# Optimization experiments

Measured on AMD Instinct MI355X. Metric: run time of the kernel, lower is better.

## Reference

```python
import jax, jax.numpy as jnp
import numpy as np

N_NODES = 100000


def gcn_conv(x, edge_index, W, b):
    # PyG GCNConv: add self-loops, sym-normalize, linear, scatter-add aggregate
    n = x.shape[0]
    loop = jnp.arange(n, dtype=edge_index.dtype)
    src = jnp.concatenate([edge_index[0], loop])  # [E+N]
    dst = jnp.concatenate([edge_index[1], loop])
    deg = jax.ops.segment_sum(jnp.ones_like(dst, dtype=x.dtype), dst, num_segments=n)
    dinv = jnp.where(deg > 0, jax.lax.rsqrt(deg), 0.0)
    h = x @ W                               # [N, out]
    norm = dinv[src] * dinv[dst]            # [E+N]
    msg = h[src] * norm[:, None]            # [E+N, out]
    out = jax.ops.segment_sum(msg, dst, num_segments=n)
    return out + b


def setup_inputs() -> dict:
    key = jax.random.key(0)
    k1, k2, k3, k4 = jax.random.split(key, 4)
    x = jax.random.normal(k1, (N_NODES, 128), dtype=jnp.float32)
    edge_index = jax.random.randint(k2, (2, 3200000), 0, N_NODES, dtype=jnp.int64)
    W1 = jax.random.normal(k3, (128, 64), dtype=jnp.float32) * (1.0 / np.sqrt(128))
    b1 = jnp.zeros((64,), dtype=jnp.float32)
    W2 = jax.random.normal(k4, (64, 2), dtype=jnp.float32) * (1.0 / np.sqrt(64))
    b2 = jnp.zeros((2,), dtype=jnp.float32)
    return {"x": x, "edge_index": edge_index, "W1": W1, "b1": b1, "W2": W2, "b2": b2}


def reference(x, edge_index, W1, b1, W2, b2):
    h = jax.nn.relu(gcn_conv(x, edge_index, W1, b1))
    return gcn_conv(h, edge_index, W2, b2)
```

## Files before the change

kernel.cpp:

```cpp
#include <hip/hip_runtime.h>
#include <hip/hip_bf16.h>
#include <math.h>

#define N_FEAT 128
#define H1 64
#define H2 2
#define BSHIFT 9
#define BWID (1 << BSHIFT)
#define EPB 8192
#define GR 32

typedef unsigned long long u64;
typedef unsigned int u32;

__device__ __forceinline__ unsigned short f2bf(float f) {
    u32 u = __float_as_uint(f);
    u += 0x7fff + ((u >> 16) & 1);
    return (unsigned short)(u >> 16);
}
__device__ __forceinline__ float bf_lo(u32 v) { return __uint_as_float(v << 16); }
__device__ __forceinline__ float bf_hi(u32 v) { return __uint_as_float(v & 0xffff0000u); }

__device__ __forceinline__ int load_idx(const void* E, size_t i, int is64) {
    if (is64) return (int)((const long long*)E)[i];
    return ((const int*)E)[i];
}

__device__ __forceinline__ int detect_is64(const void* E) {
    const u64* E64 = (const u64*)E;
    return (E64[0] <= 1000000ULL) && (E64[1] <= 1000000ULL) &&
           (E64[2] <= 1000000ULL) && (E64[3] <= 1000000ULL);
}

__global__ __launch_bounds__(256) void k_bcount(const void* __restrict__ E, size_t nE,
                                                int* __restrict__ bcnt, int NB) {
    __shared__ int hist[256];
    __shared__ int s_is64;
    int tid = threadIdx.x;
    hist[tid] = 0;
    if (tid == 0) s_is64 = detect_is64(E);
    __syncthreads();
    int is64 = s_is64;
    size_t e0 = (size_t)blockIdx.x * EPB;
    int cnt = (int)min((size_t)EPB, nE - e0);
    for (int k = tid; k < cnt; k += 256) {
        int d = load_idx(E, nE + e0 + k, is64);
        atomicAdd(&hist[d >> BSHIFT], 1);
    }
    __syncthreads();
    if (tid < NB && hist[tid]) atomicAdd(&bcnt[tid], hist[tid]);
}

__global__ void k_bscan(const int* __restrict__ bcnt, int* __restrict__ boff,
                        u32* __restrict__ gcur, int* __restrict__ rp,
                        int N, int NB, int nE) {
    __shared__ int s[1024];
    int t = threadIdx.x;
    int own = (t < NB) ? bcnt[t] : 0;
    s[t] = own;
    __syncthreads();
    for (int off = 1; off < 1024; off <<= 1) {
        int v = (t >= off) ? s[t - off] : 0;
        __syncthreads();
        s[t] += v;
        __syncthreads();
    }
    int excl = s[t] - own;
    if (t < NB) {
        boff[t] = excl;
        gcur[t] = (u32)excl;
    }
    if (t == 0) {
        boff[NB] = nE;
        rp[N] = nE;
    }
}

__global__ __launch_bounds__(256) void k_bin(const void* __restrict__ E, size_t nE,
                                             u32* __restrict__ gcur,
                                             u32* __restrict__ packed) {
    __shared__ u32 hist[256], lbase[256], lcur[256];
    __shared__ int s_is64;
    int tid = threadIdx.x;
    hist[tid] = 0;
    if (tid == 0) s_is64 = detect_is64(E);
    __syncthreads();
    int is64 = s_is64;
    size_t e0 = (size_t)blockIdx.x * EPB;
    int cnt = (int)min((size_t)EPB, nE - e0);
    for (int k = tid; k < cnt; k += 256) {
        int d = load_idx(E, nE + e0 + k, is64);
        atomicAdd(&hist[d >> BSHIFT], 1u);
    }
    __syncthreads();
    u32 h = hist[tid];
    lbase[tid] = h ? atomicAdd(&gcur[tid], h) : 0u;
    lcur[tid] = 0u;
    __syncthreads();
    for (int k = tid; k < cnt; k += 256) {
        int s = load_idx(E, e0 + k, is64);
        int d = load_idx(E, nE + e0 + k, is64);
        int b = d >> BSHIFT;
        u32 r = atomicAdd(&lcur[b], 1u);
        packed[(size_t)lbase[b] + r] = ((u32)(d & (BWID - 1)) << 17) | (u32)s;
    }
}

__global__ __launch_bounds__(512) void k_csr(const u32* __restrict__ packed,
                                             const int* __restrict__ boff,
                                             int* __restrict__ rp,
                                             float* __restrict__ dinv,
                                             int* __restrict__ col, int N) {
    __shared__ int cnt[BWID];
    __shared__ int cur[BWID];
    __shared__ int s[BWID];
    int tid = threadIdx.x;
    int b = blockIdx.x;
    cnt[tid] = 0;
    __syncthreads();
    int e0 = boff[b], e1 = boff[b + 1];
    for (int e = e0 + tid; e < e1; e += BWID)
        atomicAdd(&cnt[packed[e] >> 17], 1);
    __syncthreads();
    int own = cnt[tid];
    s[tid] = own;
    __syncthreads();
    for (int off = 1; off < BWID; off <<= 1) {
        int v = (tid >= off) ? s[tid - off] : 0;
        __syncthreads();
        s[tid] += v;
        __syncthreads();
    }
    int excl = s[tid] - own;
    int node = b * BWID + tid;
    if (node < N) {
        rp[node] = e0 + excl;
        dinv[node] = rsqrtf((float)(own + 1));
    }
    cur[tid] = excl;
    __syncthreads();
    for (int e = e0 + tid; e < e1; e += BWID) {
        u32 p = packed[e];
        int pos = e0 + atomicAdd(&cur[p >> 17], 1);
        col[pos] = (int)(p & 0x1FFFF);
    }
}

__global__ __launch_bounds__(256) void k_gemm1(const float* __restrict__ x,
                                               const float* __restrict__ W1,
                                               const float* __restrict__ dinv,
                                               unsigned short* __restrict__ h1b, int N) {
    __shared__ float Ws[N_FEAT * H1];
    __shared__ float Xs[GR * N_FEAT];
    int tid = threadIdx.x;
    for (int t = tid; t < N_FEAT * H1 / 4; t += 256)
        ((float4*)Ws)[t] = ((const float4*)W1)[t];
    int row_base = blockIdx.x * GR;
    int nrow = min(GR, N - row_base);
    const float4* xg = (const float4*)(x + (size_t)row_base * N_FEAT);
    int nf4 = nrow * (N_FEAT / 4);
    for (int t = tid; t < nf4; t += 256)
        ((float4*)Xs)[t] = xg[t];
    __syncthreads();

    int lane = tid & 63, wv = tid >> 6;
    int r0 = wv * 8;
    const float4* Xs4 = (const float4*)Xs;
    float acc[8] = {0.f, 0.f, 0.f, 0.f, 0.f, 0.f, 0.f, 0.f};
#pragma unroll 2
    for (int kk = 0; kk < N_FEAT / 4; ++kk) {
        float w0 = Ws[(4 * kk + 0) * H1 + lane];
        float w1 = Ws[(4 * kk + 1) * H1 + lane];
        float w2 = Ws[(4 * kk + 2) * H1 + lane];
        float w3 = Ws[(4 * kk + 3) * H1 + lane];
#pragma unroll
        for (int r = 0; r < 8; ++r) {
            float4 xv = Xs4[(r0 + r) * (N_FEAT / 4) + kk];
            acc[r] = fmaf(xv.x, w0, fmaf(xv.y, w1, fmaf(xv.z, w2, fmaf(xv.w, w3, acc[r]))));
        }
    }
#pragma unroll
    for (int r = 0; r < 8; ++r) {
        int row = row_base + r0 + r;
        if (row < N) h1b[(size_t)row * H1 + lane] = f2bf(acc[r] * dinv[row]);
    }
}

__global__ __launch_bounds__(256) void k_agg1(const u32* __restrict__ h1b32,
                                              const int* __restrict__ rp,
                                              const int* __restrict__ col,
                                              const float* __restrict__ dinv,
                                              const float* __restrict__ b1,
                                              const float* __restrict__ W2,
                                              float2* __restrict__ h2s, int N) {
    int node = blockIdx.x * 4 + (threadIdx.x >> 6);
    int lane = threadIdx.x & 63;
    if (node >= N) return;
    int c2 = lane & 31;
    int h = lane >> 5;
    float a0 = 0.f, a1 = 0.f;
    int e0 = rp[node], e1 = rp[node + 1];
    int deg = e1 - e0;
    int pairs = deg >> 1;
    int p = 0;
    for (; p + 8 <= pairs; p += 8) {
        int idx[8];
        u32 vv[8];
#pragma unroll
        for (int i = 0; i < 8; ++i) idx[i] = col[e0 + 2 * (p + i) + h];
#pragma unroll
        for (int i = 0; i < 8; ++i) vv[i] = h1b32[(size_t)idx[i] * 32 + c2];
#pragma unroll
        for (int i = 0; i < 8; ++i) { a0 += bf_lo(vv[i]); a1 += bf_hi(vv[i]); }
    }
    for (; p < pairs; ++p) {
        int s = col[e0 + 2 * p + h];
        u32 v = h1b32[(size_t)s * 32 + c2];
        a0 += bf_lo(v);
        a1 += bf_hi(v);
    }
    if ((deg & 1) && h == 0) {
        int s = col[e1 - 1];
        u32 v = h1b32[(size_t)s * 32 + c2];
        a0 += bf_lo(v);
        a1 += bf_hi(v);
    }
    a0 += __shfl_xor(a0, 32);
    a1 += __shfl_xor(a1, 32);
    u32 sv = h1b32[(size_t)node * 32 + c2];
    a0 += bf_lo(sv);
    a1 += bf_hi(sv);

    float di = dinv[node];
    float2 bb = ((const float2*)b1)[c2];
    float v0 = fmaxf(fmaf(di, a0, bb.x), 0.f);
    float v1 = fmaxf(fmaf(di, a1, bb.y), 0.f);
    float4 w = ((const float4*)W2)[c2];
    float p0 = fmaf(v0, w.x, v1 * w.z);
    float p1 = fmaf(v0, w.y, v1 * w.w);
#pragma unroll
    for (int off = 16; off; off >>= 1) {
        p0 += __shfl_xor(p0, off);
        p1 += __shfl_xor(p1, off);
    }
    if (lane == 0) h2s[node] = make_float2(di * p0, di * p1);
}

__global__ __launch_bounds__(256) void k_agg2(const float2* __restrict__ h2s,
                                              const int* __restrict__ rp,
                                              const int* __restrict__ col,
                                              const float* __restrict__ dinv,
                                              const float* __restrict__ b2,
                                              float2* __restrict__ out, int N) {
    int g = threadIdx.x >> 4;
    int lane = threadIdx.x & 15;
    int node = blockIdx.x * 16 + g;
    if (node >= N) return;
    int e0 = rp[node], e1 = rp[node + 1];
    float a0 = 0.f, a1 = 0.f;
    for (int e = e0 + lane; e < e1; e += 16) {
        float2 v = h2s[col[e]];
        a0 += v.x;
        a1 += v.y;
    }
#pragma unroll
    for (int off = 8; off; off >>= 1) {
        a0 += __shfl_xor(a0, off, 16);
        a1 += __shfl_xor(a1, off, 16);
    }
    if (lane == 0) {
        float di = dinv[node];
        float2 self = h2s[node];
        out[node] = make_float2(fmaf(di, a0 + self.x, b2[0]),
                                fmaf(di, a1 + self.y, b2[1]));
    }
}

extern "C" void kernel_launch(void* const* d_in, const int* in_sizes, int n_in,
                              void* d_out, int out_size, void* d_ws, size_t ws_size,
                              hipStream_t stream) {
    const float* x  = (const float*)d_in[0];
    const void*  E  = d_in[1];
    const float* W1 = (const float*)d_in[2];
    const float* b1 = (const float*)d_in[3];
    const float* W2 = (const float*)d_in[4];
    const float* b2 = (const float*)d_in[5];
    float2* out = (float2*)d_out;

    const int N  = in_sizes[0] / N_FEAT;
    const int nE = in_sizes[1] / 2;
    const int NB = (N + BWID - 1) / BWID;

    char* ws = (char*)d_ws;
    size_t off = 0;
    auto alloc = [&](size_t bytes) -> void* {
        void* p = ws + off;
        off = (off + bytes + 255) & ~(size_t)255;
        return p;
    };
    int*            bcnt   = (int*)alloc((size_t)NB * 4);
    int*            boff   = (int*)alloc((size_t)(NB + 1) * 4);
    u32*            gcur   = (u32*)alloc((size_t)NB * 4);
    int*            rp     = (int*)alloc((size_t)(N + 1) * 4);
    float*          dinv   = (float*)alloc((size_t)N * 4);
    int*            col    = (int*)alloc((size_t)nE * 4);
    u32*            packed = (u32*)alloc((size_t)nE * 4);
    unsigned short* h1b    = (unsigned short*)alloc((size_t)N * H1 * 2);
    float2*         h2s    = (float2*)alloc((size_t)N * 8);

    hipMemsetAsync(bcnt, 0, (size_t)NB * 4, stream);

    const int cgrid = (nE + EPB - 1) / EPB;

    k_bcount<<<cgrid, 256, 0, stream>>>(E, (size_t)nE, bcnt, NB);
    k_bscan<<<1, 1024, 0, stream>>>(bcnt, boff, gcur, rp, N, NB, nE);
    k_bin<<<cgrid, 256, 0, stream>>>(E, (size_t)nE, gcur, packed);
    k_csr<<<NB, BWID, 0, stream>>>(packed, boff, rp, dinv, col, N);
    k_gemm1<<<(N + GR - 1) / GR, 256, 0, stream>>>(x, W1, dinv, h1b, N);
    k_agg1<<<(N + 3) / 4, 256, 0, stream>>>((const u32*)h1b, rp, col, dinv, b1, W2, h2s, N);
    k_agg2<<<(N + 15) / 16, 256, 0, stream>>>(h2s, rp, col, dinv, b2, out, N);
}
```

Measured before the change: 325.6 us.

## Use 16-byte gathers with 8 edges per wave in agg1; wave-shuffle scan in CSR

The layer-1 aggregation now has each lane load a uint4 (8 bf16 channels), so a 64-lane wave gathers 8 neighbor rows at once instead of 2. Each lane keeps 8 accumulators, and the partial sums are reduced across lane groups with shuffles before the bias, ReLU and W2 projection. The CSR kernel's block-wide Hillis-Steele scan, which needed many __syncthreads, is replaced by a per-wave shuffle scan plus a small shared-memory pass over wave totals. The wider gathers are meant to cut load instructions and expose more memory parallelism, at the cost of more registers and shuffle work per node and a change in summation order.

```diff
diff --git a/kernel.cpp b/kernel.cpp
--- a/kernel.cpp
+++ b/kernel.cpp
@@ -113,8 +113,9 @@
                                              int* __restrict__ col, int N) {
     __shared__ int cnt[BWID];
     __shared__ int cur[BWID];
-    __shared__ int s[BWID];
+    __shared__ int wsum[8];
     int tid = threadIdx.x;
+    int lane = tid & 63, wv = tid >> 6;
     int b = blockIdx.x;
     cnt[tid] = 0;
     __syncthreads();
@@ -123,15 +124,18 @@
         atomicAdd(&cnt[packed[e] >> 17], 1);
     __syncthreads();
     int own = cnt[tid];
-    s[tid] = own;
-    __syncthreads();
-    for (int off = 1; off < BWID; off <<= 1) {
-        int v = (tid >= off) ? s[tid - off] : 0;
-        __syncthreads();
-        s[tid] += v;
-        __syncthreads();
-    }
-    int excl = s[tid] - own;
+    int v = own;
+#pragma unroll
+    for (int off = 1; off < 64; off <<= 1) {
+        int t = __shfl_up(v, off);
+        if (lane >= off) v += t;
+    }
+    if (lane == 63) wsum[wv] = v;
+    __syncthreads();
+    int add = 0;
+#pragma unroll
+    for (int w = 0; w < 8; ++w) add += (w < wv) ? wsum[w] : 0;
+    int excl = v + add - own;
     int node = b * BWID + tid;
     if (node < N) {
         rp[node] = e0 + excl;
@@ -186,7 +190,7 @@
     }
 }
 
-__global__ __launch_bounds__(256) void k_agg1(const u32* __restrict__ h1b32,
+__global__ __launch_bounds__(256) void k_agg1(const uint4* __restrict__ h1q,
                                               const int* __restrict__ rp,
                                               const int* __restrict__ col,
                                               const float* __restrict__ dinv,
@@ -196,50 +200,67 @@
     int node = blockIdx.x * 4 + (threadIdx.x >> 6);
     int lane = threadIdx.x & 63;
     if (node >= N) return;
-    int c2 = lane & 31;
-    int h = lane >> 5;
-    float a0 = 0.f, a1 = 0.f;
+    int g = lane >> 3;
+    int c4 = lane & 7;
+    float acc[8] = {0.f, 0.f, 0.f, 0.f, 0.f, 0.f, 0.f, 0.f};
     int e0 = rp[node], e1 = rp[node + 1];
-    int deg = e1 - e0;
-    int pairs = deg >> 1;
-    int p = 0;
-    for (; p + 8 <= pairs; p += 8) {
-        int idx[8];
-        u32 vv[8];
-#pragma unroll
-        for (int i = 0; i < 8; ++i) idx[i] = col[e0 + 2 * (p + i) + h];
-#pragma unroll
-        for (int i = 0; i < 8; ++i) vv[i] = h1b32[(size_t)idx[i] * 32 + c2];
-#pragma unroll
-        for (int i = 0; i < 8; ++i) { a0 += bf_lo(vv[i]); a1 += bf_hi(vv[i]); }
-    }
-    for (; p < pairs; ++p) {
-        int s = col[e0 + 2 * p + h];
-        u32 v = h1b32[(size_t)s * 32 + c2];
-        a0 += bf_lo(v);
-        a1 += bf_hi(v);
-    }
-    if ((deg & 1) && h == 0) {
-        int s = col[e1 - 1];
-        u32 v = h1b32[(size_t)s * 32 + c2];
-        a0 += bf_lo(v);
-        a1 += bf_hi(v);
-    }
-    a0 += __shfl_xor(a0, 32);
-    a1 += __shfl_xor(a1, 32);
-    u32 sv = h1b32[(size_t)node * 32 + c2];
-    a0 += bf_lo(sv);
-    a1 += bf_hi(sv);
-
+    int e = e0 + g;
+    for (; e + 24 < e1; e += 32) {
+        int s0 = col[e], s1 = col[e + 8], s2 = col[e + 16], s3 = col[e + 24];
+        uint4 v0 = h1q[(size_t)s0 * 8 + c4];
+        uint4 v1 = h1q[(size_t)s1 * 8 + c4];
+        uint4 v2 = h1q[(size_t)s2 * 8 + c4];
+        uint4 v3 = h1q[(size_t)s3 * 8 + c4];
+        acc[0] += bf_lo(v0.x) + bf_lo(v1.x) + bf_lo(v2.x) + bf_lo(v3.x);
+        acc[1] += bf_hi(v0.x) + bf_hi(v1.x) + bf_hi(v2.x) + bf_hi(v3.x);
+        acc[2] += bf_lo(v0.y) + bf_lo(v1.y) + bf_lo(v2.y) + bf_lo(v3.y);
+        acc[3] += bf_hi(v0.y) + bf_hi(v1.y) + bf_hi(v2.y) + bf_hi(v3.y);
+        acc[4] += bf_lo(v0.z) + bf_lo(v1.z) + bf_lo(v2.z) + bf_lo(v3.z);
+        acc[5] += bf_hi(v0.z) + bf_hi(v1.z) + bf_hi(v2.z) + bf_hi(v3.z);
+        acc[6] += bf_lo(v0.w) + bf_lo(v1.w) + bf_lo(v2.w) + bf_lo(v3.w);
+        acc[7] += bf_hi(v0.w) + bf_hi(v1.w) + bf_hi(v2.w) + bf_hi(v3.w);
+    }
+    for (; e < e1; e += 8) {
+        int s = col[e];
+        uint4 v = h1q[(size_t)s * 8 + c4];
+        acc[0] += bf_lo(v.x); acc[1] += bf_hi(v.x);
+        acc[2] += bf_lo(v.y); acc[3] += bf_hi(v.y);
+        acc[4] += bf_lo(v.z); acc[5] += bf_hi(v.z);
+        acc[6] += bf_lo(v.w); acc[7] += bf_hi(v.w);
+    }
+#pragma unroll
+    for (int off = 8; off < 64; off <<= 1) {
+#pragma unroll
+        for (int i = 0; i < 8; ++i) acc[i] += __shfl_xor(acc[i], off);
+    }
+    {
+        uint4 v = h1q[(size_t)node * 8 + c4];
+        acc[0] += bf_lo(v.x); acc[1] += bf_hi(v.x);
+        acc[2] += bf_lo(v.y); acc[3] += bf_hi(v.y);
+        acc[4] += bf_lo(v.z); acc[5] += bf_hi(v.z);
+        acc[6] += bf_lo(v.w); acc[7] += bf_hi(v.w);
+    }
     float di = dinv[node];
-    float2 bb = ((const float2*)b1)[c2];
-    float v0 = fmaxf(fmaf(di, a0, bb.x), 0.f);
-    float v1 = fmaxf(fmaf(di, a1, bb.y), 0.f);
-    float4 w = ((const float4*)W2)[c2];
-    float p0 = fmaf(v0, w.x, v1 * w.z);
-    float p1 = fmaf(v0, w.y, v1 * w.w);
-#pragma unroll
-    for (int off = 16; off; off >>= 1) {
+    float4 bA = ((const float4*)b1)[c4 * 2 + 0];
+    float4 bB = ((const float4*)b1)[c4 * 2 + 1];
+    float vch[8];
+    vch[0] = fmaxf(fmaf(di, acc[0], bA.x), 0.f);
+    vch[1] = fmaxf(fmaf(di, acc[1], bA.y), 0.f);
+    vch[2] = fmaxf(fmaf(di, acc[2], bA.z), 0.f);
+    vch[3] = fmaxf(fmaf(di, acc[3], bA.w), 0.f);
+    vch[4] = fmaxf(fmaf(di, acc[4], bB.x), 0.f);
+    vch[5] = fmaxf(fmaf(di, acc[5], bB.y), 0.f);
+    vch[6] = fmaxf(fmaf(di, acc[6], bB.z), 0.f);
+    vch[7] = fmaxf(fmaf(di, acc[7], bB.w), 0.f);
+    float p0 = 0.f, p1 = 0.f;
+#pragma unroll
+    for (int q = 0; q < 4; ++q) {
+        float4 w = ((const float4*)W2)[c4 * 4 + q];
+        p0 += vch[2 * q] * w.x + vch[2 * q + 1] * w.z;
+        p1 += vch[2 * q] * w.y + vch[2 * q + 1] * w.w;
+    }
+#pragma unroll
+    for (int off = 1; off < 8; off <<= 1) {
         p0 += __shfl_xor(p0, off);
         p1 += __shfl_xor(p1, off);
     }
@@ -317,6 +338,6 @@
     k_bin<<<cgrid, 256, 0, stream>>>(E, (size_t)nE, gcur, packed);
     k_csr<<<NB, BWID, 0, stream>>>(packed, boff, rp, dinv, col, N);
     k_gemm1<<<(N + GR - 1) / GR, 256, 0, stream>>>(x, W1, dinv, h1b, N);
-    k_agg1<<<(N + 3) / 4, 256, 0, stream>>>((const u32*)h1b, rp, col, dinv, b1, W2, h2s, N);
+    k_agg1<<<(N + 3) / 4, 256, 0, stream>>>((const uint4*)h1b, rp, col, dinv, b1, W2, h2s, N);
     k_agg2<<<(N + 15) / 16, 256, 0, stream>>>(h2s, rp, col, dinv, b2, out, N);
 }
```

New measurement: 310.4 us. 4.7% less time.
